# Kernel tuning notes

Measured on AMD Instinct MI355X. Metric: run time of the kernel, lower is better.

The kernel has to match this reference:

```python
import jax, jax.numpy as jnp
import numpy as np

# 16-joint kinematic tree (index 0 = root); child i depends on PARENTS[i]
PARENTS = [0, 0, 1, 2, 3, 1, 5, 6, 1, 8, 9, 10, 8, 12, 13, 14]
NUM_LAYERS = 2
H = 1024          # output_size = input_size + bridge_size
B = 256           # batch
D = 512           # input_size == bridge_size


def setup_inputs() -> dict:
    key = jax.random.key(0)
    ks = jax.random.split(key, 6)
    n_nodes = len(PARENTS) - 1  # 15 non-root joints
    s = 1.0 / np.sqrt(H).astype(np.float32)  # torch LSTM init scale
    return {
        "input": jax.random.normal(ks[0], (n_nodes, B, D), jnp.float32),
        "bridge": jax.random.normal(ks[1], (n_nodes, B, D), jnp.float32),
        "W_ih": jax.random.normal(ks[2], (NUM_LAYERS, 4 * H, H), jnp.float32) * s,
        "W_hh": jax.random.normal(ks[3], (NUM_LAYERS, 4 * H, H), jnp.float32) * s,
        "b_ih": jax.random.normal(ks[4], (NUM_LAYERS, 4 * H), jnp.float32) * s,
        "b_hh": jax.random.normal(ks[5], (NUM_LAYERS, 4 * H), jnp.float32) * s,
    }


def _lstm_cell(x, h, c, Wih, Whh, bih, bhh):
    # gates: [B, 4H], torch gate order i, f, g, o
    g = x @ Wih.T + h @ Whh.T + (bih + bhh)
    i, f, gg, o = jnp.split(g, 4, axis=-1)
    c_new = jax.nn.sigmoid(f) * c + jax.nn.sigmoid(i) * jnp.tanh(gg)
    h_new = jax.nn.sigmoid(o) * jnp.tanh(c_new)
    return h_new, c_new


def reference(input, bridge, W_ih, W_hh, b_ih, b_hh):
    # batch_first=False: inputs are [n_nodes, B, D]; concat -> feature H = 2D
    x_all = jnp.concatenate([input, bridge], axis=-1)   # [n_nodes, B, H]
    x_all = jnp.transpose(x_all, (1, 0, 2))             # [B, n_nodes, H]
    batch = x_all.shape[0]
    zero = jnp.zeros((NUM_LAYERS, batch, H), x_all.dtype)
    hs, cs = [zero], [zero]  # root joint starts with zero state
    outs = []
    # serial walk over the fixed, small kinematic tree (15 joints)
    for j in range(1, len(PARENTS)):
        ph, pc = hs[PARENTS[j]], cs[PARENTS[j]]
        x = x_all[:, j - 1]
        new_h, new_c = [], []
        for l in range(NUM_LAYERS):
            h, c = _lstm_cell(x, ph[l], pc[l], W_ih[l], W_hh[l], b_ih[l], b_hh[l])
            new_h.append(h)
            new_c.append(c)
            x = h  # top layer output feeds next layer / becomes joint output
        outs.append(x)
        hs.append(jnp.stack(new_h))
        cs.append(jnp.stack(new_c))
    out = jnp.stack(outs, axis=1)          # [B, n_nodes, H]
    return jnp.transpose(out, (1, 0, 2))   # back to seq-first [n_nodes, B, H]
```

## Files before the change

kernel.cpp:

```cpp
#include <hip/hip_runtime.h>
#include <stdint.h>

typedef unsigned short u16;
typedef uint32_t u32;
typedef short s16x8 __attribute__((ext_vector_type(8)));
typedef float fx16 __attribute__((ext_vector_type(16)));

#define B_   256
#define H_   1024
#define BH_  (B_ * H_)
#define WPE  ((size_t)2 * 4096 * 2048)
#define XPE  ((size_t)15 * BH_)
#define HPE  ((size_t)32 * BH_)
#define NT   32

struct Stage { int node[8]; int par[8]; int layer[8]; int cnt; };

__device__ __forceinline__ u16 bf16_rn(float x) {
    union { float f; u32 u; } v; v.f = x;
    return (u16)((v.u + 0x7FFFu + ((v.u >> 16) & 1u)) >> 16);
}
__device__ __forceinline__ float sigf(float x) {
    return __builtin_amdgcn_rcpf(1.0f + __expf(-x));
}
__device__ __forceinline__ float tanh_f(float x) {
    return 1.0f - 2.0f * __builtin_amdgcn_rcpf(1.0f + __expf(2.0f * x));
}

__global__ __launch_bounds__(256)
void pack_weights(const float* __restrict__ Wih, const float* __restrict__ Whh,
                  u16* __restrict__ wp)
{
    const int gt = blockIdx.x * 256 + threadIdx.x;
    const int w = gt >> 6, lane = gt & 63;
    const int k16 = w & 127, cg = (w >> 7) & 31, gate = (w >> 12) & 3, layer = w >> 14;
    const int row = gate * 1024 + cg * 32 + (lane & 31);
    const int k = k16 * 16 + (lane >> 5) * 8;
    const float* src = (k < 1024)
        ? Wih + ((size_t)layer * 4096 + row) * 1024 + k
        : Whh + ((size_t)layer * 4096 + row) * 1024 + (k - 1024);
    const float4 v0 = *(const float4*)src;
    const float4 v1 = *(const float4*)(src + 4);
    const float a[8] = {v0.x, v0.y, v0.z, v0.w, v1.x, v1.y, v1.z, v1.w};
    union { u16 s[8]; uint4 v; } hi;
    #pragma unroll
    for (int e = 0; e < 8; ++e) hi.s[e] = bf16_rn(a[e]);
    *(uint4*)(wp + (size_t)w * 512 + (size_t)lane * 8) = hi.v;
}

__global__ __launch_bounds__(256)
void pack_x(const float* __restrict__ input, const float* __restrict__ bridge,
            u16* __restrict__ xp)
{
    const int gt = blockIdx.x * 256 + threadIdx.x;
    const int w = gt >> 6, lane = gt & 63;
    const int k16 = w & 63, btile = (w >> 6) & 7, n1 = w >> 9;
    const int b = btile * 32 + (lane & 31);
    const int k = k16 * 16 + (lane >> 5) * 8;
    const float* src = (k < 512)
        ? input  + ((size_t)n1 * 256 + b) * 512 + k
        : bridge + ((size_t)n1 * 256 + b) * 512 + (k - 512);
    const float4 v0 = *(const float4*)src;
    const float4 v1 = *(const float4*)(src + 4);
    const float a[8] = {v0.x, v0.y, v0.z, v0.w, v1.x, v1.y, v1.z, v1.w};
    union { u16 s[8]; uint4 v; } hi;
    #pragma unroll
    for (int e = 0; e < 8; ++e) hi.s[e] = bf16_rn(a[e]);
    *(uint4*)(xp + (size_t)w * 512 + (size_t)lane * 8) = hi.v;
}

__global__ __launch_bounds__(256)
void bias_sum_k(const float* __restrict__ bih, const float* __restrict__ bhh,
                float* __restrict__ bs)
{
    const int i = blockIdx.x * 256 + threadIdx.x;
    if (i < 8192) bs[i] = bih[i] + bhh[i];
}

__global__ __launch_bounds__(256, 3)
void cell_fused(const u16* __restrict__ wp, const u16* __restrict__ xp,
                u16* __restrict__ hp, float* __restrict__ c_buf,
                const float* __restrict__ bsum, float* __restrict__ out,
                Stage st)
{
    __shared__ __align__(16) char SMEM[37376];
    u16*   AL   = (u16*)SMEM;
    u16*   WL   = AL + 8192;
    float* gbuf = (float*)SMEM;
    u16*   tbuf = (u16*)(SMEM + 33024);

    const int u = blockIdx.x;
    const int hhblk = 4 * (u & 7) + ((u >> 3) & 3);
    const int v = u >> 5;
    const int cnt = st.cnt;
    const int cell = v % cnt;
    const int mblk = v / cnt;
    const int node = st.node[cell], par = st.par[cell], layer = st.layer[cell];
    const int tid = threadIdx.x, wv = tid >> 6, lane = tid & 63;
    const int mw = wv >> 1, nw = wv & 1;
    const int tg = tid >> 6;
    const int tl8 = (tid & 63) * 8;

    const u16 *A0, *A1;
    if (layer == 0) {
        A0 = xp + (size_t)(node - 1) * BH_;
        A1 = hp + (size_t)(par * 2 + 0) * BH_;
    } else {
        A0 = hp + (size_t)(node * 2 + 0) * BH_;
        A1 = hp + (size_t)(par * 2 + 1) * BH_;
    }
    size_t wsrc[4];
    #pragma unroll
    for (int g = 0; g < 4; ++g)
        wsrc[g] = ((size_t)((layer * 4 + g) * 32 + hhblk) * 128 + tg) * 512
                + (size_t)tl8;

    fx16 acc[2][2];
    #pragma unroll
    for (int m = 0; m < 2; ++m)
        #pragma unroll
        for (int n = 0; n < 2; ++n)
            #pragma unroll
            for (int r = 0; r < 16; ++r) acc[m][n][r] = 0.0f;

    #pragma unroll 1
    for (int t = 0; t < NT; ++t) {
        const u16* As = (t < 16) ? A0 : A1;
        const int k16 = (t & 15) * 4 + tg;
        #pragma unroll
        for (int i = 0; i < 4; ++i) {
            __builtin_amdgcn_global_load_lds(
                (const __attribute__((address_space(1))) void*)
                    (As + ((size_t)(mblk * 4 + i) * 64 + k16) * 512 + tl8),
                (__attribute__((address_space(3))) void*)
                    (AL + (i * 4 + tg) * 512 + tl8),
                16, 0, 0);
        }
        #pragma unroll
        for (int i = 0; i < 4; ++i) {
            __builtin_amdgcn_global_load_lds(
                (const __attribute__((address_space(1))) void*)
                    (wp + wsrc[i] + (size_t)t * 4 * 512),
                (__attribute__((address_space(3))) void*)
                    (WL + (i * 4 + tg) * 512 + tl8),
                16, 0, 0);
        }
        __syncthreads();
        #pragma unroll
        for (int kk = 0; kk < 4; ++kk) {
            s16x8 a[2], w[2];
            #pragma unroll
            for (int m = 0; m < 2; ++m)
                a[m] = *(const s16x8*)(AL + ((mw * 2 + m) * 4 + kk) * 512 + lane * 8);
            #pragma unroll
            for (int n = 0; n < 2; ++n)
                w[n] = *(const s16x8*)(WL + ((nw * 2 + n) * 4 + kk) * 512 + lane * 8);
            #pragma unroll
            for (int m = 0; m < 2; ++m)
                #pragma unroll
                for (int n = 0; n < 2; ++n)
                    acc[m][n] = __builtin_amdgcn_mfma_f32_32x32x16_bf16(
                        a[m], w[n], acc[m][n], 0, 0, 0);
        }
        __syncthreads();
    }

    const int hhl  = tid & 31;
    const int colg = hhblk * 32 + hhl;
    float bs4[4];
    #pragma unroll
    for (int g = 0; g < 4; ++g)
        bs4[g] = bsum[layer * 4096 + g * 1024 + colg];

    const float* cpar = c_buf + (size_t)(par * 2 + layer) * BH_ + colg;
    float*       cnew = c_buf + (size_t)(node * 2 + layer) * BH_ + colg;
    float*       outp = out + (size_t)(node - 1) * BH_ + colg;
    u16*         hpn  = hp + (size_t)(node * 2 + layer) * BH_;

    #pragma unroll
    for (int p = 0; p < 2; ++p) {
        __syncthreads();
        if (mw == p) {
            #pragma unroll
            for (int m = 0; m < 2; ++m) {
                #pragma unroll
                for (int n = 0; n < 2; ++n) {
                    const int col = (nw * 2 + n) * 32 + (lane & 31);
                    #pragma unroll
                    for (int r = 0; r < 16; ++r) {
                        const int row_l = m * 32 + 4 * (lane >> 5)
                                        + (r & 3) + 8 * (r >> 2);
                        gbuf[row_l * 129 + col] = acc[m][n][r];
                    }
                }
            }
        }
        __syncthreads();
        #pragma unroll
        for (int e = 0; e < 8; ++e) {
            const int row_l = e * 8 + (tid >> 5);
            const size_t grow = (size_t)(mblk * 128 + p * 64 + row_l) * 1024;
            const float gi = gbuf[row_l * 129 + 0  * 32 + hhl] + bs4[0];
            const float gf = gbuf[row_l * 129 + 1  * 32 + hhl] + bs4[1];
            const float gg = gbuf[row_l * 129 + 2  * 32 + hhl] + bs4[2];
            const float go = gbuf[row_l * 129 + 3  * 32 + hhl] + bs4[3];
            const float cp = cpar[grow];
            const float cn = sigf(gf) * cp + sigf(gi) * tanh_f(gg);
            const float hn = sigf(go) * tanh_f(cn);
            cnew[grow] = cn;
            if (layer == 1) outp[grow] = hn;
            tbuf[row_l * 33 + hhl] = bf16_rn(hn);
        }
        __syncthreads();
        {
            const int j = wv >> 1, q = wv & 1;
            const int bt   = mblk * 4 + p * 2 + j;
            const int k16h = hhblk * 2 + q;
            union { u16 s[8]; uint4 v; } pk;
            #pragma unroll
            for (int e = 0; e < 8; ++e)
                pk.s[e] = tbuf[(j * 32 + (lane & 31)) * 33
                               + q * 16 + (lane >> 5) * 8 + e];
            *(uint4*)(hpn + ((size_t)bt * 64 + k16h) * 512 + lane * 8) = pk.v;
        }
    }
}

extern "C" void kernel_launch(void* const* d_in, const int* in_sizes, int n_in,
                              void* d_out, int out_size, void* d_ws, size_t ws_size,
                              hipStream_t stream)
{
    const float* input  = (const float*)d_in[0];
    const float* bridge = (const float*)d_in[1];
    const float* Wih    = (const float*)d_in[2];
    const float* Whh    = (const float*)d_in[3];
    const float* bih    = (const float*)d_in[4];
    const float* bhh    = (const float*)d_in[5];
    float* out = (float*)d_out;

    u16* wp = (u16*)d_ws;
    u16* xp = wp + WPE;
    u16* hp = xp + XPE;
    float* c_buf = (float*)(hp + HPE);
    float* bsum  = c_buf + HPE;

    hipMemsetAsync(hp, 0, (size_t)2 * BH_ * sizeof(u16), stream);
    hipMemsetAsync(c_buf, 0, (size_t)2 * BH_ * sizeof(float), stream);

    bias_sum_k<<<32, 256, 0, stream>>>(bih, bhh, bsum);
    pack_weights<<<8192, 256, 0, stream>>>(Wih, Whh, wp);
    pack_x<<<1920, 256, 0, stream>>>(input, bridge, xp);

    static const Stage stages[7] = {
        { {1},                      {0},                      {0},                      1 },
        { {1,2,5,8},                {0,1,1,1},                {1,0,0,0},                4 },
        { {2,5,8,3,6,9,12},         {1,1,1,2,5,8,8},          {1,1,1,0,0,0,0},          7 },
        { {3,6,9,12,4,7,10,13},     {2,5,8,8,3,6,9,12},       {1,1,1,1,0,0,0,0},        8 },
        { {4,7,10,13,11,14},        {3,6,9,12,10,13},         {1,1,1,1,0,0},            6 },
        { {11,14,15},               {10,13,14},               {1,1,0},                  3 },
        { {15},                     {14},                     {1},                      1 },
    };

    for (int s = 0; s < 7; ++s) {
        cell_fused<<<dim3(stages[s].cnt * 64), 256, 0, stream>>>(
            wp, xp, hp, c_buf, bsum, out, stages[s]);
    }
}
```

Before: 297.5 us.

## Add split-K GEMM with separate gate reduction for narrow stages; double-buffer LDS

```diff
diff --git a/kernel.cpp b/kernel.cpp
--- a/kernel.cpp
+++ b/kernel.cpp
@@ -13,6 +13,7 @@
 #define XPE  ((size_t)15 * BH_)
 #define HPE  ((size_t)32 * BH_)
 #define NT   32
+#define GPLANE ((size_t)B_ * 4096)
 
 struct Stage { int node[8]; int par[8]; int layer[8]; int cnt; };
 
@@ -77,24 +78,23 @@
     if (i < 8192) bs[i] = bih[i] + bhh[i];
 }
 
-__global__ __launch_bounds__(256, 3)
+__global__ __launch_bounds__(256, 2)
 void cell_fused(const u16* __restrict__ wp, const u16* __restrict__ xp,
                 u16* __restrict__ hp, float* __restrict__ c_buf,
                 const float* __restrict__ bsum, float* __restrict__ out,
                 Stage st)
 {
-    __shared__ __align__(16) char SMEM[37376];
-    u16*   AL   = (u16*)SMEM;
-    u16*   WL   = AL + 8192;
+    __shared__ __align__(16) char SMEM[65536];
+    u16*   BUF  = (u16*)SMEM;
     float* gbuf = (float*)SMEM;
     u16*   tbuf = (u16*)(SMEM + 33024);
 
-    const int u = blockIdx.x;
-    const int hhblk = 4 * (u & 7) + ((u >> 3) & 3);
-    const int v = u >> 5;
-    const int cnt = st.cnt;
-    const int cell = v % cnt;
-    const int mblk = v / cnt;
+    const int bid  = blockIdx.x;
+    const int half = gridDim.x >> 1;
+    const int mblk = (bid >= half) ? 1 : 0;
+    const int v    = bid - mblk * half;
+    const int hhblk = 4 * (v & 7) + ((v >> 3) & 3);
+    const int cell  = v >> 5;
     const int node = st.node[cell], par = st.par[cell], layer = st.layer[cell];
     const int tid = threadIdx.x, wv = tid >> 6, lane = tid & 63;
     const int mw = wv >> 1, nw = wv & 1;
@@ -115,6 +115,50 @@
         wsrc[g] = ((size_t)((layer * 4 + g) * 32 + hhblk) * 128 + tg) * 512
                 + (size_t)tl8;
 
+    #define STAGE(T, BB) do {                                                  \
+        const u16* As_ = ((T) < 16) ? A0 : A1;                                 \
+        const int k16_ = ((T) & 15) * 4 + tg;                                  \
+        _Pragma("unroll")                                                      \
+        for (int i_ = 0; i_ < 4; ++i_) {                                       \
+            __builtin_amdgcn_global_load_lds(                                  \
+                (const __attribute__((address_space(1))) void*)                \
+                    (As_ + ((size_t)(mblk * 4 + i_) * 64 + k16_) * 512 + tl8), \
+                (__attribute__((address_space(3))) void*)                      \
+                    (BUF + (BB) * 16384 + (i_ * 4 + tg) * 512 + tl8),          \
+                16, 0, 0);                                                     \
+        }                                                                      \
+        _Pragma("unroll")                                                      \
+        for (int i_ = 0; i_ < 4; ++i_) {                                       \
+            __builtin_amdgcn_global_load_lds(                                  \
+                (const __attribute__((address_space(1))) void*)                \
+                    (wp + wsrc[i_] + (size_t)(T) * 2048),                      \
+                (__attribute__((address_space(3))) void*)                      \
+                    (BUF + (BB) * 16384 + 8192 + (i_ * 4 + tg) * 512 + tl8),   \
+                16, 0, 0);                                                     \
+        }                                                                      \
+    } while (0)
+
+    #define COMPUTE(BB) do {                                                   \
+        _Pragma("unroll")                                                      \
+        for (int kk_ = 0; kk_ < 4; ++kk_) {                                    \
+            s16x8 a_[2], w_[2];                                                \
+            _Pragma("unroll")                                                  \
+            for (int m_ = 0; m_ < 2; ++m_)                                     \
+                a_[m_] = *(const s16x8*)(BUF + (BB) * 16384                    \
+                        + ((mw * 2 + m_) * 4 + kk_) * 512 + lane * 8);         \
+            _Pragma("unroll")                                                  \
+            for (int n_ = 0; n_ < 2; ++n_)                                     \
+                w_[n_] = *(const s16x8*)(BUF + (BB) * 16384 + 8192             \
+                        + ((nw * 2 + n_) * 4 + kk_) * 512 + lane * 8);         \
+            _Pragma("unroll")                                                  \
+            for (int m_ = 0; m_ < 2; ++m_)                                     \
+                _Pragma("unroll")                                              \
+                for (int n_ = 0; n_ < 2; ++n_)                                 \
+                    acc[m_][n_] = __builtin_amdgcn_mfma_f32_32x32x16_bf16(     \
+                        a_[m_], w_[n_], acc[m_][n_], 0, 0, 0);                 \
+        }                                                                      \
+    } while (0)
+
     fx16 acc[2][2];
     #pragma unroll
     for (int m = 0; m < 2; ++m)
@@ -123,46 +167,12 @@
             #pragma unroll
             for (int r = 0; r < 16; ++r) acc[m][n][r] = 0.0f;
 
+    STAGE(0, 0);
     #pragma unroll 1
     for (int t = 0; t < NT; ++t) {
-        const u16* As = (t < 16) ? A0 : A1;
-        const int k16 = (t & 15) * 4 + tg;
-        #pragma unroll
-        for (int i = 0; i < 4; ++i) {
-            __builtin_amdgcn_global_load_lds(
-                (const __attribute__((address_space(1))) void*)
-                    (As + ((size_t)(mblk * 4 + i) * 64 + k16) * 512 + tl8),
-                (__attribute__((address_space(3))) void*)
-                    (AL + (i * 4 + tg) * 512 + tl8),
-                16, 0, 0);
-        }
-        #pragma unroll
-        for (int i = 0; i < 4; ++i) {
-            __builtin_amdgcn_global_load_lds(
-                (const __attribute__((address_space(1))) void*)
-                    (wp + wsrc[i] + (size_t)t * 4 * 512),
-                (__attribute__((address_space(3))) void*)
-                    (WL + (i * 4 + tg) * 512 + tl8),
-                16, 0, 0);
-        }
         __syncthreads();
-        #pragma unroll
-        for (int kk = 0; kk < 4; ++kk) {
-            s16x8 a[2], w[2];
-            #pragma unroll
-            for (int m = 0; m < 2; ++m)
-                a[m] = *(const s16x8*)(AL + ((mw * 2 + m) * 4 + kk) * 512 + lane * 8);
-            #pragma unroll
-            for (int n = 0; n < 2; ++n)
-                w[n] = *(const s16x8*)(WL + ((nw * 2 + n) * 4 + kk) * 512 + lane * 8);
-            #pragma unroll
-            for (int m = 0; m < 2; ++m)
-                #pragma unroll
-                for (int n = 0; n < 2; ++n)
-                    acc[m][n] = __builtin_amdgcn_mfma_f32_32x32x16_bf16(
-                        a[m], w[n], acc[m][n], 0, 0, 0);
-        }
-        __syncthreads();
+        if (t + 1 < NT) STAGE(t + 1, (t + 1) & 1);
+        COMPUTE(t & 1);
     }
 
     const int hhl  = tid & 31;
@@ -200,10 +210,10 @@
         for (int e = 0; e < 8; ++e) {
             const int row_l = e * 8 + (tid >> 5);
             const size_t grow = (size_t)(mblk * 128 + p * 64 + row_l) * 1024;
-            const float gi = gbuf[row_l * 129 + 0  * 32 + hhl] + bs4[0];
-            const float gf = gbuf[row_l * 129 + 1  * 32 + hhl] + bs4[1];
-            const float gg = gbuf[row_l * 129 + 2  * 32 + hhl] + bs4[2];
-            const float go = gbuf[row_l * 129 + 3  * 32 + hhl] + bs4[3];
+            const float gi = gbuf[row_l * 129 + 0 * 32 + hhl] + bs4[0];
+            const float gf = gbuf[row_l * 129 + 1 * 32 + hhl] + bs4[1];
+            const float gg = gbuf[row_l * 129 + 2 * 32 + hhl] + bs4[2];
+            const float go = gbuf[row_l * 129 + 3 * 32 + hhl] + bs4[3];
             const float cp = cpar[grow];
             const float cn = sigf(gf) * cp + sigf(gi) * tanh_f(gg);
             const float hn = sigf(go) * tanh_f(cn);
@@ -224,6 +234,186 @@
             *(uint4*)(hpn + ((size_t)bt * 64 + k16h) * 512 + lane * 8) = pk.v;
         }
     }
+    #undef STAGE
+    #undef COMPUTE
+}
+
+__global__ __launch_bounds__(256, 2)
+void cell_gemm_sk(const u16* __restrict__ wp, const u16* __restrict__ xp,
+                  const u16* __restrict__ hp, float* __restrict__ gpart,
+                  Stage st, int S, int NTs)
+{
+    __shared__ __align__(16) char SMEM[65536];
+    u16* BUF = (u16*)SMEM;
+
+    const int bid  = blockIdx.x;
+    const int per  = 64 * S;
+    const int cell = bid / per;
+    const int rr   = bid % per;
+    const int sp   = rr >> 6;
+    const int u    = rr & 63;
+    const int hhblk = 4 * (u & 7) + ((u >> 3) & 3);
+    const int mblk  = u >> 5;
+    const int node = st.node[cell], par = st.par[cell], layer = st.layer[cell];
+    const int tid = threadIdx.x, wv = tid >> 6, lane = tid & 63;
+    const int mw = wv >> 1, nw = wv & 1;
+    const int tg = tid >> 6;
+    const int tl8 = (tid & 63) * 8;
+
+    const u16 *A0, *A1;
+    if (layer == 0) {
+        A0 = xp + (size_t)(node - 1) * BH_;
+        A1 = hp + (size_t)(par * 2 + 0) * BH_;
+    } else {
+        A0 = hp + (size_t)(node * 2 + 0) * BH_;
+        A1 = hp + (size_t)(par * 2 + 1) * BH_;
+    }
+    size_t wsrc[4];
+    #pragma unroll
+    for (int g = 0; g < 4; ++g)
+        wsrc[g] = ((size_t)((layer * 4 + g) * 32 + hhblk) * 128 + tg) * 512
+                + (size_t)tl8;
+
+    #define STAGE(T, BB) do {                                                  \
+        const u16* As_ = ((T) < 16) ? A0 : A1;                                 \
+        const int k16_ = ((T) & 15) * 4 + tg;                                  \
+        _Pragma("unroll")                                                      \
+        for (int i_ = 0; i_ < 4; ++i_) {                                       \
+            __builtin_amdgcn_global_load_lds(                                  \
+                (const __attribute__((address_space(1))) void*)                \
+                    (As_ + ((size_t)(mblk * 4 + i_) * 64 + k16_) * 512 + tl8), \
+                (__attribute__((address_space(3))) void*)                      \
+                    (BUF + (BB) * 16384 + (i_ * 4 + tg) * 512 + tl8),          \
+                16, 0, 0);                                                     \
+        }                                                                      \
+        _Pragma("unroll")                                                      \
+        for (int i_ = 0; i_ < 4; ++i_) {                                       \
+            __builtin_amdgcn_global_load_lds(                                  \
+                (const __attribute__((address_space(1))) void*)                \
+                    (wp + wsrc[i_] + (size_t)(T) * 2048),                      \
+                (__attribute__((address_space(3))) void*)                      \
+                    (BUF + (BB) * 16384 + 8192 + (i_ * 4 + tg) * 512 + tl8),   \
+                16, 0, 0);                                                     \
+        }                                                                      \
+    } while (0)
+
+    #define COMPUTE(BB) do {                                                   \
+        _Pragma("unroll")                                                      \
+        for (int kk_ = 0; kk_ < 4; ++kk_) {                                    \
+            s16x8 a_[2], w_[2];                                                \
+            _Pragma("unroll")                                                  \
+            for (int m_ = 0; m_ < 2; ++m_)                                     \
+                a_[m_] = *(const s16x8*)(BUF + (BB) * 16384                    \
+                        + ((mw * 2 + m_) * 4 + kk_) * 512 + lane * 8);         \
+            _Pragma("unroll")                                                  \
+            for (int n_ = 0; n_ < 2; ++n_)                                     \
+                w_[n_] = *(const s16x8*)(BUF + (BB) * 16384 + 8192             \
+                        + ((nw * 2 + n_) * 4 + kk_) * 512 + lane * 8);         \
+            _Pragma("unroll")                                                  \
+            for (int m_ = 0; m_ < 2; ++m_)                                     \
+                _Pragma("unroll")                                              \
+                for (int n_ = 0; n_ < 2; ++n_)                                 \
+                    acc[m_][n_] = __builtin_amdgcn_mfma_f32_32x32x16_bf16(     \
+                        a_[m_], w_[n_], acc[m_][n_], 0, 0, 0);                 \
+        }                                                                      \
+    } while (0)
+
+    fx16 acc[2][2];
+    #pragma unroll
+    for (int m = 0; m < 2; ++m)
+        #pragma unroll
+        for (int n = 0; n < 2; ++n)
+            #pragma unroll
+            for (int r = 0; r < 16; ++r) acc[m][n][r] = 0.0f;
+
+    const int t0 = sp * NTs;
+    STAGE(t0, 0);
+    #pragma unroll 1
+    for (int tl = 0; tl < NTs; ++tl) {
+        __syncthreads();
+        if (tl + 1 < NTs) STAGE(t0 + tl + 1, (tl + 1) & 1);
+        COMPUTE(tl & 1);
+    }
+
+    float* gp = gpart + (size_t)(cell * S + sp) * GPLANE
+              + (size_t)(mblk * 128) * 4096 + hhblk * 32 + (lane & 31);
+    #pragma unroll
+    for (int m = 0; m < 2; ++m) {
+        #pragma unroll
+        for (int n = 0; n < 2; ++n) {
+            const int gate = nw * 2 + n;
+            #pragma unroll
+            for (int r = 0; r < 16; ++r) {
+                const int row = mw * 64 + m * 32 + 4 * (lane >> 5)
+                              + (r & 3) + 8 * (r >> 2);
+                gp[(size_t)row * 4096 + gate * 1024] = acc[m][n][r];
+            }
+        }
+    }
+    #undef STAGE
+    #undef COMPUTE
+}
+
+__global__ __launch_bounds__(256)
+void gates_red(const float* __restrict__ gpart, const float* __restrict__ bsum,
+               float* __restrict__ c_buf, u16* __restrict__ hp,
+               float* __restrict__ out, Stage st, int S)
+{
+    __shared__ u16 tbuf[128 * 33];
+
+    const int u = blockIdx.x;
+    const int cell = blockIdx.y;
+    const int hhblk = 4 * (u & 7) + ((u >> 3) & 3);
+    const int mblk  = u >> 5;
+    const int node = st.node[cell], par = st.par[cell], layer = st.layer[cell];
+    const int tid = threadIdx.x, wv = tid >> 6, lane = tid & 63;
+    const int hhl = tid & 31, rg = tid >> 5;
+    const int colg = hhblk * 32 + hhl;
+
+    float bs4[4];
+    #pragma unroll
+    for (int g = 0; g < 4; ++g)
+        bs4[g] = bsum[layer * 4096 + g * 1024 + colg];
+
+    const float* cpar = c_buf + (size_t)(par * 2 + layer) * BH_ + colg;
+    float*       cnew = c_buf + (size_t)(node * 2 + layer) * BH_ + colg;
+    float*       outp = out + (size_t)(node - 1) * BH_ + colg;
+    u16*         hpn  = hp + (size_t)(node * 2 + layer) * BH_;
+    const float* gpc  = gpart + (size_t)cell * S * GPLANE;
+
+    #pragma unroll 1
+    for (int it = 0; it < 16; ++it) {
+        const int row_l = it * 8 + rg;
+        const size_t grow = (size_t)(mblk * 128 + row_l);
+        float gv[4];
+        #pragma unroll
+        for (int g = 0; g < 4; ++g) {
+            float s = bs4[g];
+            #pragma unroll 1
+            for (int sp = 0; sp < S; ++sp)
+                s += gpc[(size_t)sp * GPLANE + grow * 4096 + g * 1024 + colg];
+            gv[g] = s;
+        }
+        const float cp = cpar[grow * 1024];
+        const float cn = sigf(gv[1]) * cp + sigf(gv[0]) * tanh_f(gv[2]);
+        const float hn = sigf(gv[3]) * tanh_f(cn);
+        cnew[grow * 1024] = cn;
+        if (layer == 1) outp[grow * 1024] = hn;
+        tbuf[row_l * 33 + hhl] = bf16_rn(hn);
+    }
+    __syncthreads();
+
+    #pragma unroll
+    for (int q = 0; q < 2; ++q) {
+        const int bt   = mblk * 4 + wv;
+        const int k16h = hhblk * 2 + q;
+        union { u16 s[8]; uint4 v; } pk;
+        #pragma unroll
+        for (int e = 0; e < 8; ++e)
+            pk.s[e] = tbuf[(wv * 32 + (lane & 31)) * 33
+                           + q * 16 + (lane >> 5) * 8 + e];
+        *(uint4*)(hpn + ((size_t)bt * 64 + k16h) * 512 + lane * 8) = pk.v;
+    }
 }
 
 extern "C" void kernel_launch(void* const* d_in, const int* in_sizes, int n_in,
@@ -243,6 +433,7 @@
     u16* hp = xp + XPE;
     float* c_buf = (float*)(hp + HPE);
     float* bsum  = c_buf + HPE;
+    float* gpart = bsum + 8192;
 
     hipMemsetAsync(hp, 0, (size_t)2 * BH_ * sizeof(u16), stream);
     hipMemsetAsync(c_buf, 0, (size_t)2 * BH_ * sizeof(float), stream);
@@ -260,9 +451,20 @@
         { {11,14,15},               {10,13,14},               {1,1,0},                  3 },
         { {15},                     {14},                     {1},                      1 },
     };
+    static const int use_sk[7] = {1, 1, 0, 0, 0, 1, 1};
+    static const int splits[7] = {4, 2, 0, 0, 0, 2, 4};
 
     for (int s = 0; s < 7; ++s) {
-        cell_fused<<<dim3(stages[s].cnt * 64), 256, 0, stream>>>(
-            wp, xp, hp, c_buf, bsum, out, stages[s]);
-    }
-}
+        const Stage& st = stages[s];
+        if (use_sk[s]) {
+            const int S = splits[s];
+            cell_gemm_sk<<<dim3(st.cnt * 64 * S), 256, 0, stream>>>(
+                wp, xp, hp, gpart, st, S, NT / S);
+            gates_red<<<dim3(64, st.cnt), 256, 0, stream>>>(
+                gpart, bsum, c_buf, hp, out, st, S);
+        } else {
+            cell_fused<<<dim3(st.cnt * 64), 256, 0, stream>>>(
+                wp, xp, hp, c_buf, bsum, out, st);
+        }
+    }
+}
```

Measured after the change: 465.4 us. +56.4%, slower.

## Load MFMA operands directly from global to registers, skip zero parent-state half

Applied to the files above, without the earlier changes.

```diff
diff --git a/kernel.cpp b/kernel.cpp
--- a/kernel.cpp
+++ b/kernel.cpp
@@ -77,29 +77,26 @@
     if (i < 8192) bs[i] = bih[i] + bhh[i];
 }
 
-__global__ __launch_bounds__(256, 3)
+__global__ __launch_bounds__(256, 2)
 void cell_fused(const u16* __restrict__ wp, const u16* __restrict__ xp,
                 u16* __restrict__ hp, float* __restrict__ c_buf,
                 const float* __restrict__ bsum, float* __restrict__ out,
                 Stage st)
 {
     __shared__ __align__(16) char SMEM[37376];
-    u16*   AL   = (u16*)SMEM;
-    u16*   WL   = AL + 8192;
     float* gbuf = (float*)SMEM;
     u16*   tbuf = (u16*)(SMEM + 33024);
 
-    const int u = blockIdx.x;
-    const int hhblk = 4 * (u & 7) + ((u >> 3) & 3);
-    const int v = u >> 5;
-    const int cnt = st.cnt;
-    const int cell = v % cnt;
-    const int mblk = v / cnt;
+    const int bid  = blockIdx.x;
+    const int half = gridDim.x >> 1;
+    const int mblk = (bid >= half) ? 1 : 0;
+    const int v    = bid - mblk * half;
+    const int hhblk = 4 * (v & 7) + ((v >> 3) & 3);
+    const int cell  = v >> 5;
     const int node = st.node[cell], par = st.par[cell], layer = st.layer[cell];
     const int tid = threadIdx.x, wv = tid >> 6, lane = tid & 63;
     const int mw = wv >> 1, nw = wv & 1;
-    const int tg = tid >> 6;
-    const int tl8 = (tid & 63) * 8;
+    const int l8 = lane * 8;
 
     const u16 *A0, *A1;
     if (layer == 0) {
@@ -109,11 +106,19 @@
         A0 = hp + (size_t)(node * 2 + 0) * BH_;
         A1 = hp + (size_t)(par * 2 + 1) * BH_;
     }
-    size_t wsrc[4];
-    #pragma unroll
-    for (int g = 0; g < 4; ++g)
-        wsrc[g] = ((size_t)((layer * 4 + g) * 32 + hhblk) * 128 + tg) * 512
-                + (size_t)tl8;
+    const u16* a0s[2]; const u16* a1s[2];
+    #pragma unroll
+    for (int m = 0; m < 2; ++m) {
+        const size_t bt = (size_t)(mblk * 4 + mw * 2 + m) * 64 * 512 + l8;
+        a0s[m] = A0 + bt;
+        a1s[m] = A1 + bt;
+    }
+    const u16* wns[2];
+    #pragma unroll
+    for (int n = 0; n < 2; ++n)
+        wns[n] = wp + (size_t)((layer * 4 + (nw * 2 + n)) * 32 + hhblk) * 65536 + l8;
+
+    const int nsteps = (par == 0) ? (NT / 2) : NT;
 
     fx16 acc[2][2];
     #pragma unroll
@@ -123,46 +128,35 @@
             #pragma unroll
             for (int r = 0; r < 16; ++r) acc[m][n][r] = 0.0f;
 
-    #pragma unroll 1
-    for (int t = 0; t < NT; ++t) {
-        const u16* As = (t < 16) ? A0 : A1;
-        const int k16 = (t & 15) * 4 + tg;
-        #pragma unroll
-        for (int i = 0; i < 4; ++i) {
-            __builtin_amdgcn_global_load_lds(
-                (const __attribute__((address_space(1))) void*)
-                    (As + ((size_t)(mblk * 4 + i) * 64 + k16) * 512 + tl8),
-                (__attribute__((address_space(3))) void*)
-                    (AL + (i * 4 + tg) * 512 + tl8),
-                16, 0, 0);
-        }
-        #pragma unroll
-        for (int i = 0; i < 4; ++i) {
-            __builtin_amdgcn_global_load_lds(
-                (const __attribute__((address_space(1))) void*)
-                    (wp + wsrc[i] + (size_t)t * 4 * 512),
-                (__attribute__((address_space(3))) void*)
-                    (WL + (i * 4 + tg) * 512 + tl8),
-                16, 0, 0);
-        }
-        __syncthreads();
-        #pragma unroll
-        for (int kk = 0; kk < 4; ++kk) {
-            s16x8 a[2], w[2];
-            #pragma unroll
-            for (int m = 0; m < 2; ++m)
-                a[m] = *(const s16x8*)(AL + ((mw * 2 + m) * 4 + kk) * 512 + lane * 8);
-            #pragma unroll
-            for (int n = 0; n < 2; ++n)
-                w[n] = *(const s16x8*)(WL + ((nw * 2 + n) * 4 + kk) * 512 + lane * 8);
+    #pragma unroll 2
+    for (int t = 0; t < nsteps; ++t) {
+        const int seg1 = (t >= 16);
+        const size_t ka = (size_t)((t & 15) * 4) * 512;
+        const size_t kw = (size_t)(t * 4) * 512;
+
+        s16x8 a[2][4], w[2][4];
+        #pragma unroll
+        for (int m = 0; m < 2; ++m) {
+            const u16* ap = (seg1 ? a1s[m] : a0s[m]) + ka;
+            #pragma unroll
+            for (int kk = 0; kk < 4; ++kk)
+                a[m][kk] = *(const s16x8*)(ap + (size_t)kk * 512);
+        }
+        #pragma unroll
+        for (int n = 0; n < 2; ++n) {
+            const u16* wpn = wns[n] + kw;
+            #pragma unroll
+            for (int kk = 0; kk < 4; ++kk)
+                w[n][kk] = *(const s16x8*)(wpn + (size_t)kk * 512);
+        }
+        #pragma unroll
+        for (int kk = 0; kk < 4; ++kk)
             #pragma unroll
             for (int m = 0; m < 2; ++m)
                 #pragma unroll
                 for (int n = 0; n < 2; ++n)
                     acc[m][n] = __builtin_amdgcn_mfma_f32_32x32x16_bf16(
-                        a[m], w[n], acc[m][n], 0, 0, 0);
-        }
-        __syncthreads();
+                        a[m][kk], w[n][kk], acc[m][n], 0, 0, 0);
     }
 
     const int hhl  = tid & 31;
```

New measurement: 346.5 us. 16.5% more time.

## Double-buffer LDS tiles with async loads and skip zero-state hidden GEMM

Applied to the files above, without the earlier changes.

```diff
diff --git a/kernel.cpp b/kernel.cpp
--- a/kernel.cpp
+++ b/kernel.cpp
@@ -77,15 +77,14 @@
     if (i < 8192) bs[i] = bih[i] + bhh[i];
 }
 
-__global__ __launch_bounds__(256, 3)
+__global__ __launch_bounds__(256, 2)
 void cell_fused(const u16* __restrict__ wp, const u16* __restrict__ xp,
                 u16* __restrict__ hp, float* __restrict__ c_buf,
                 const float* __restrict__ bsum, float* __restrict__ out,
                 Stage st)
 {
-    __shared__ __align__(16) char SMEM[37376];
-    u16*   AL   = (u16*)SMEM;
-    u16*   WL   = AL + 8192;
+    __shared__ __align__(16) char SMEM[65536];
+    u16*   BUF  = (u16*)SMEM;
     float* gbuf = (float*)SMEM;
     u16*   tbuf = (u16*)(SMEM + 33024);
 
@@ -115,6 +114,52 @@
         wsrc[g] = ((size_t)((layer * 4 + g) * 32 + hhblk) * 128 + tg) * 512
                 + (size_t)tl8;
 
+    #define STAGE(T, BB) do {                                                  \
+        const u16* As_ = ((T) < 16) ? A0 : A1;                                 \
+        const int k16_ = ((T) & 15) * 4 + tg;                                  \
+        _Pragma("unroll")                                                      \
+        for (int i_ = 0; i_ < 4; ++i_) {                                       \
+            __builtin_amdgcn_global_load_lds(                                  \
+                (const __attribute__((address_space(1))) void*)                \
+                    (As_ + ((size_t)(mblk * 4 + i_) * 64 + k16_) * 512 + tl8), \
+                (__attribute__((address_space(3))) void*)                      \
+                    (BUF + (BB) * 16384 + (i_ * 4 + tg) * 512 + tl8),          \
+                16, 0, 0);                                                     \
+        }                                                                      \
+        _Pragma("unroll")                                                      \
+        for (int i_ = 0; i_ < 4; ++i_) {                                       \
+            __builtin_amdgcn_global_load_lds(                                  \
+                (const __attribute__((address_space(1))) void*)                \
+                    (wp + wsrc[i_] + (size_t)(T) * 2048),                      \
+                (__attribute__((address_space(3))) void*)                      \
+                    (BUF + (BB) * 16384 + 8192 + (i_ * 4 + tg) * 512 + tl8),   \
+                16, 0, 0);                                                     \
+        }                                                                      \
+    } while (0)
+
+    #define COMPUTE(BB) do {                                                   \
+        _Pragma("unroll")                                                      \
+        for (int kk_ = 0; kk_ < 4; ++kk_) {                                    \
+            s16x8 a_[2], w_[2];                                                \
+            _Pragma("unroll")                                                  \
+            for (int m_ = 0; m_ < 2; ++m_)                                     \
+                a_[m_] = *(const s16x8*)(BUF + (BB) * 16384                    \
+                        + ((mw * 2 + m_) * 4 + kk_) * 512 + lane * 8);         \
+            _Pragma("unroll")                                                  \
+            for (int n_ = 0; n_ < 2; ++n_)                                     \
+                w_[n_] = *(const s16x8*)(BUF + (BB) * 16384 + 8192             \
+                        + ((nw * 2 + n_) * 4 + kk_) * 512 + lane * 8);         \
+            _Pragma("unroll")                                                  \
+            for (int m_ = 0; m_ < 2; ++m_)                                     \
+                _Pragma("unroll")                                              \
+                for (int n_ = 0; n_ < 2; ++n_)                                 \
+                    acc[m_][n_] = __builtin_amdgcn_mfma_f32_32x32x16_bf16(     \
+                        a_[m_], w_[n_], acc[m_][n_], 0, 0, 0);                 \
+        }                                                                      \
+    } while (0)
+
+    const int nsteps = (par == 0) ? (NT / 2) : NT;
+
     fx16 acc[2][2];
     #pragma unroll
     for (int m = 0; m < 2; ++m)
@@ -123,47 +168,22 @@
             #pragma unroll
             for (int r = 0; r < 16; ++r) acc[m][n][r] = 0.0f;
 
+    STAGE(0, 0);
+    STAGE(1, 1);
+
     #pragma unroll 1
-    for (int t = 0; t < NT; ++t) {
-        const u16* As = (t < 16) ? A0 : A1;
-        const int k16 = (t & 15) * 4 + tg;
-        #pragma unroll
-        for (int i = 0; i < 4; ++i) {
-            __builtin_amdgcn_global_load_lds(
-                (const __attribute__((address_space(1))) void*)
-                    (As + ((size_t)(mblk * 4 + i) * 64 + k16) * 512 + tl8),
-                (__attribute__((address_space(3))) void*)
-                    (AL + (i * 4 + tg) * 512 + tl8),
-                16, 0, 0);
-        }
-        #pragma unroll
-        for (int i = 0; i < 4; ++i) {
-            __builtin_amdgcn_global_load_lds(
-                (const __attribute__((address_space(1))) void*)
-                    (wp + wsrc[i] + (size_t)t * 4 * 512),
-                (__attribute__((address_space(3))) void*)
-                    (WL + (i * 4 + tg) * 512 + tl8),
-                16, 0, 0);
-        }
-        __syncthreads();
-        #pragma unroll
-        for (int kk = 0; kk < 4; ++kk) {
-            s16x8 a[2], w[2];
-            #pragma unroll
-            for (int m = 0; m < 2; ++m)
-                a[m] = *(const s16x8*)(AL + ((mw * 2 + m) * 4 + kk) * 512 + lane * 8);
-            #pragma unroll
-            for (int n = 0; n < 2; ++n)
-                w[n] = *(const s16x8*)(WL + ((nw * 2 + n) * 4 + kk) * 512 + lane * 8);
-            #pragma unroll
-            for (int m = 0; m < 2; ++m)
-                #pragma unroll
-                for (int n = 0; n < 2; ++n)
-                    acc[m][n] = __builtin_amdgcn_mfma_f32_32x32x16_bf16(
-                        a[m], w[n], acc[m][n], 0, 0, 0);
-        }
-        __syncthreads();
-    }
+    for (int t = 0; t < nsteps; ++t) {
+        if (t == nsteps - 1) {
+            asm volatile("s_waitcnt vmcnt(0)" ::: "memory");
+        } else {
+            asm volatile("s_waitcnt vmcnt(8)" ::: "memory");
+        }
+        __builtin_amdgcn_s_barrier();
+        COMPUTE(t & 1);
+        __builtin_amdgcn_s_barrier();
+        if (t + 2 < nsteps) STAGE(t + 2, t & 1);
+    }
+    __syncthreads();
 
     const int hhl  = tid & 31;
     const int colg = hhblk * 32 + hhl;
@@ -224,6 +244,8 @@
             *(uint4*)(hpn + ((size_t)bt * 64 + k16h) * 512 + lane * 8) = pk.v;
         }
     }
+    #undef STAGE
+    #undef COMPUTE
 }
 
 extern "C" void kernel_launch(void* const* d_in, const int* in_sizes, int n_in,
```

New measurement: 254.7 us. -14.4%, faster.
